# Kernel tuning notes

Hardware: AMD Instinct MI355X
Metric: run time of the kernel (lower is better)

The kernel has to match this reference:

```python
import jax, jax.numpy as jnp
import numpy as np

N_NODES = 50000
N_EDGES = 600000
IN_FEATS, HIDDEN, READOUT = 128, 128, 64
NUM_GRAPHS = 128
NEG_SLOPE = 0.01


def setup_inputs() -> dict:
    key = jax.random.key(0)
    ks = jax.random.split(key, 7)
    return {
        "x": jax.random.normal(ks[0], (N_NODES, IN_FEATS), dtype=jnp.float32),
        "edge_weight": jax.random.uniform(ks[1], (N_EDGES,), dtype=jnp.float32),
        "W1": jax.random.normal(ks[2], (IN_FEATS, HIDDEN), dtype=jnp.float32) * 0.05,
        "W2": jax.random.normal(ks[3], (HIDDEN, READOUT), dtype=jnp.float32) * 0.05,
        "src": jax.random.randint(ks[4], (N_EDGES,), 0, N_NODES, dtype=jnp.int32),
        "dst": jax.random.randint(ks[5], (N_EDGES,), 0, N_NODES, dtype=jnp.int32),
        "graph_ids": jax.random.randint(ks[6], (N_NODES,), 0, NUM_GRAPHS, dtype=jnp.int32),
        "num_graphs": NUM_GRAPHS,
    }


def reference(x, edge_weight, W1, W2, src, dst, graph_ids, num_graphs):
    n = x.shape[0]
    # DGL GraphConv norm='both': symmetric normalization from UNWEIGHTED degrees
    ones_e = jnp.ones(src.shape[0], dtype=x.dtype)
    out_deg = jnp.clip(jax.ops.segment_sum(ones_e, src, num_segments=n), 1.0)
    in_deg = jnp.clip(jax.ops.segment_sum(ones_e, dst, num_segments=n), 1.0)
    norm_src = out_deg ** -0.5  # applied on source side
    norm_dst = in_deg ** -0.5   # applied on destination side

    def gconv(h, W):
        # mult-W-first (in_feats >= out_feats path in DGL); math identical either way
        h = h @ W                               # [N, out]
        m = (h * norm_src[:, None])[src] * edge_weight[:, None]  # [E, out]
        agg = jax.ops.segment_sum(m, dst, num_segments=n)        # [N, out]
        return agg * norm_dst[:, None]

    h = jax.nn.leaky_relu(gconv(x, W1), NEG_SLOPE)
    h = jax.nn.leaky_relu(gconv(h, W2), NEG_SLOPE)

    # dgl.mean_nodes: per-graph mean over ragged node segments
    sums = jax.ops.segment_sum(h, graph_ids, num_segments=num_graphs)
    counts = jnp.clip(
        jax.ops.segment_sum(jnp.ones(n, dtype=h.dtype), graph_ids, num_segments=num_graphs),
        1.0,
    )
    return sums / counts[:, None]
```

## Files before the change

kernel.cpp:

```cpp
#include <hip/hip_runtime.h>


#define LB256 __launch_bounds__(256)
#define LB512 __launch_bounds__(512)

constexpr int RB = 128;
constexpr int CH = 8192;
constexpr int CHB = 13;
constexpr int SPLIT = 32;

__device__ __forceinline__ float leaky(float v) { return v > 0.f ? v : 0.01f * v; }

__global__ LB512 void k_hist(const int* __restrict__ src, const int* __restrict__ dst,
                             int* __restrict__ Pin, int* __restrict__ Pout,
                             int E, int epb) {
    __shared__ int hin[CH];
    __shared__ int hout[CH];
    const int c = blockIdx.x / SPLIT;
    const int s = blockIdx.x % SPLIT;
    const int t = threadIdx.x;
    const int4 z{0, 0, 0, 0};
    for (int i = t; i < CH / 4; i += 512) {
        ((int4*)hin)[i] = z;
        ((int4*)hout)[i] = z;
    }
    __syncthreads();

    const int base = c << CHB;
    const int e0 = s * epb;
    const int e1 = min(E, e0 + epb);
    if (e0 < e1) {
        const int nv = (e1 - e0) >> 2;
        const int4* d4 = (const int4*)(dst + e0);
        const int4* s4 = (const int4*)(src + e0);
        for (int i = t; i < nv; i += 512) {
            const int4 dd = d4[i], ss = s4[i];
            int v;
            v = dd.x - base; if ((unsigned)v < (unsigned)CH) atomicAdd(&hin[v], 1);
            v = dd.y - base; if ((unsigned)v < (unsigned)CH) atomicAdd(&hin[v], 1);
            v = dd.z - base; if ((unsigned)v < (unsigned)CH) atomicAdd(&hin[v], 1);
            v = dd.w - base; if ((unsigned)v < (unsigned)CH) atomicAdd(&hin[v], 1);
            v = ss.x - base; if ((unsigned)v < (unsigned)CH) atomicAdd(&hout[v], 1);
            v = ss.y - base; if ((unsigned)v < (unsigned)CH) atomicAdd(&hout[v], 1);
            v = ss.z - base; if ((unsigned)v < (unsigned)CH) atomicAdd(&hout[v], 1);
            v = ss.w - base; if ((unsigned)v < (unsigned)CH) atomicAdd(&hout[v], 1);
        }
        for (int e = e0 + (nv << 2) + t; e < e1; e += 512) {
            int v = dst[e] - base; if ((unsigned)v < (unsigned)CH) atomicAdd(&hin[v], 1);
            v = src[e] - base;     if ((unsigned)v < (unsigned)CH) atomicAdd(&hout[v], 1);
        }
    }
    __syncthreads();

    int4* pi = (int4*)&Pin[((size_t)c * SPLIT + s) * CH];
    int4* po = (int4*)&Pout[((size_t)c * SPLIT + s) * CH];
    for (int i = t; i < CH / 4; i += 512) {
        pi[i] = ((const int4*)hin)[i];
        po[i] = ((const int4*)hout)[i];
    }
}

__global__ LB256 void k_hreduce(int* __restrict__ Pin, const int* __restrict__ Pout,
                                int* __restrict__ cin, float* __restrict__ nin,
                                float* __restrict__ nout, int N) {
    const int i = blockIdx.x * 256 + threadIdx.x;
    if (i >= N) return;
    const int c = i >> CHB, l = i & (CH - 1);
    const size_t base = (size_t)c * SPLIT * CH + l;
    int acc = 0;
#pragma unroll
    for (int s = 0; s < SPLIT; ++s) {
        const size_t idx = base + (size_t)s * CH;
        const int v = Pin[idx];
        Pin[idx] = acc;
        acc += v;
    }
    int ao = 0;
#pragma unroll
    for (int s = 0; s < SPLIT; ++s) ao += Pout[base + (size_t)s * CH];
    cin[i] = acc;
    nin[i]  = rsqrtf(fmaxf((float)acc, 1.f));
    nout[i] = rsqrtf(fmaxf((float)ao, 1.f));
}

__device__ __forceinline__ int block_scan_incl(int v, int t) {
    const int lane = t & 63, w = t >> 6;
#pragma unroll
    for (int off = 1; off < 64; off <<= 1) {
        int n = __shfl_up(v, off);
        if (lane >= off) v += n;
    }
    __shared__ int wsum[4];
    if (lane == 63) wsum[w] = v;
    __syncthreads();
    int base = 0;
#pragma unroll
    for (int k = 0; k < 4; ++k)
        if (k < w) base += wsum[k];
    return v + base;
}

__global__ LB256 void k_scan1(const int* __restrict__ cnt, int* __restrict__ excl,
                              int* __restrict__ bsum, int N) {
    const int t = threadIdx.x, i = blockIdx.x * 256 + t;
    const int orig = (i < N) ? cnt[i] : 0;
    const int incl = block_scan_incl(orig, t);
    if (i < N) excl[i] = incl - orig;
    if (t == 255) bsum[blockIdx.x] = incl;
}

__global__ LB256 void k_scan2(const int* __restrict__ bsum, int* __restrict__ boff, int NB) {
    const int t = threadIdx.x;
    const int orig = (t < NB) ? bsum[t] : 0;
    const int incl = block_scan_incl(orig, t);
    if (t < NB) boff[t] = incl - orig;
}

__global__ LB256 void k_scan3(const int* __restrict__ excl, const int* __restrict__ boff,
                              int* __restrict__ row_off, int N) {
    const int i = blockIdx.x * 256 + threadIdx.x;
    if (i < N) row_off[i] = excl[i] + boff[blockIdx.x];
}

__global__ LB512 void k_fillr(const int* __restrict__ src, const int* __restrict__ dst,
                              const float* __restrict__ ew, const float* __restrict__ nout,
                              const int* __restrict__ Pin, const int* __restrict__ row_off,
                              int2* __restrict__ srw, int E, int epb) {
    __shared__ int h[CH];
    const int c = blockIdx.x / SPLIT;
    const int s = blockIdx.x % SPLIT;
    const int t = threadIdx.x;
    const int4 z{0, 0, 0, 0};
    for (int i = t; i < CH / 4; i += 512) ((int4*)h)[i] = z;
    __syncthreads();

    const int base = c << CHB;
    const int e0 = s * epb;
    const int e1 = min(E, e0 + epb);
    const int* off = &Pin[((size_t)c * SPLIT + s) * CH];
    if (e0 < e1) {
        const int nv = (e1 - e0) >> 2;
        const int4* d4 = (const int4*)(dst + e0);
        const int4* s4 = (const int4*)(src + e0);
        const float4* w4 = (const float4*)(ew + e0);
        for (int i = t; i < nv; i += 512) {
            const int4 dd = d4[i], ss = s4[i];
            const float4 ww = w4[i];
#define FILL1(D, S, W)                                                       \
            {                                                                \
                const int dl = (D) - base;                                   \
                if ((unsigned)dl < (unsigned)CH) {                           \
                    const int r = atomicAdd(&h[dl], 1);                      \
                    const int pos = row_off[D] + off[dl] + r;                \
                    srw[pos] = make_int2((S), __float_as_int(nout[S] * (W)));\
                }                                                            \
            }
            FILL1(dd.x, ss.x, ww.x)
            FILL1(dd.y, ss.y, ww.y)
            FILL1(dd.z, ss.z, ww.z)
            FILL1(dd.w, ss.w, ww.w)
        }
        for (int e = e0 + (nv << 2) + t; e < e1; e += 512) {
            FILL1(dst[e], src[e], ew[e])
        }
#undef FILL1
    }
}

template <int BN, int TN>
__global__ LB256 void k_gemm(const float* __restrict__ A, const float* __restrict__ W,
                             float* __restrict__ C, int N, int K) {
    constexpr int BM = 64, BK = 32;
    __shared__ float Xs[BM][BK + 1];
    __shared__ float Ws[BK][BN];

    const int tid = threadIdx.x;
    const int r0 = blockIdx.x * BM;
    const int ty = tid >> 4;
    const int tx = tid & 15;

    float acc[4][TN];
#pragma unroll
    for (int i = 0; i < 4; ++i)
#pragma unroll
        for (int j = 0; j < TN; ++j) acc[i][j] = 0.f;

    const int lrow = tid >> 2;
    const int lc = (tid & 3) * 4;
    const int kr = tid >> 3;

    for (int kc = 0; kc < K; kc += BK) {
        const int gr = r0 + lrow;
        if (gr < N) {
            *(float4*)&Xs[lrow][lc]      = *(const float4*)&A[(size_t)gr * K + kc + lc];
            *(float4*)&Xs[lrow][lc + 16] = *(const float4*)&A[(size_t)gr * K + kc + lc + 16];
        } else {
            *(float4*)&Xs[lrow][lc]      = float4{0.f, 0.f, 0.f, 0.f};
            *(float4*)&Xs[lrow][lc + 16] = float4{0.f, 0.f, 0.f, 0.f};
        }
#pragma unroll
        for (int j = 0; j < BN / 32; ++j) {
            const int c4 = (tid & 7) + j * 8;
            *(float4*)&Ws[kr][c4 * 4] =
                *(const float4*)&W[(size_t)(kc + kr) * BN + c4 * 4];
        }
        __syncthreads();

#pragma unroll
        for (int k = 0; k < BK; ++k) {
            float xv[4];
#pragma unroll
            for (int i = 0; i < 4; ++i) xv[i] = Xs[ty * 4 + i][k];
            float wv[TN];
#pragma unroll
            for (int j4 = 0; j4 < TN / 4; ++j4) {
                const float4 w4 = *(const float4*)&Ws[k][tx * TN + j4 * 4];
                wv[j4 * 4 + 0] = w4.x; wv[j4 * 4 + 1] = w4.y;
                wv[j4 * 4 + 2] = w4.z; wv[j4 * 4 + 3] = w4.w;
            }
#pragma unroll
            for (int i = 0; i < 4; ++i)
#pragma unroll
                for (int j = 0; j < TN; ++j) acc[i][j] = fmaf(xv[i], wv[j], acc[i][j]);
        }
        __syncthreads();
    }

#pragma unroll
    for (int i = 0; i < 4; ++i) {
        const int r = r0 + ty * 4 + i;
        if (r < N) {
#pragma unroll
            for (int j4 = 0; j4 < TN / 4; ++j4) {
                float4 o{acc[i][j4 * 4 + 0], acc[i][j4 * 4 + 1],
                         acc[i][j4 * 4 + 2], acc[i][j4 * 4 + 3]};
                *(float4*)&C[(size_t)r * BN + tx * TN + j4 * 4] = o;
            }
        }
    }
}

template <int F, int LANES>
__global__ LB256 void k_agg(const int* __restrict__ row_off, const int* __restrict__ cnt,
                            const int2* __restrict__ srw, const float* __restrict__ nin,
                            const float* __restrict__ h, float* __restrict__ out, int N) {
    const int node = blockIdx.x * (256 / LANES) + threadIdx.x / LANES;
    if (node >= N) return;
    const int lane = threadIdx.x % LANES;
    const int start = row_off[node], len = cnt[node];

    float4 accA{0.f, 0.f, 0.f, 0.f}, accB{0.f, 0.f, 0.f, 0.f};
    int j = 0;
    for (; j + 3 < len; j += 4) {
        const int b = start + j;
        const int2 r0_ = srw[b + 0], r1_ = srw[b + 1], r2_ = srw[b + 2], r3_ = srw[b + 3];
        const float c0 = __int_as_float(r0_.y), c1 = __int_as_float(r1_.y);
        const float c2 = __int_as_float(r2_.y), c3 = __int_as_float(r3_.y);
        const float4 v0 = *(const float4*)&h[(size_t)r0_.x * F + lane * 4];
        const float4 v1 = *(const float4*)&h[(size_t)r1_.x * F + lane * 4];
        const float4 v2 = *(const float4*)&h[(size_t)r2_.x * F + lane * 4];
        const float4 v3 = *(const float4*)&h[(size_t)r3_.x * F + lane * 4];
        accA.x = fmaf(c0, v0.x, fmaf(c1, v1.x, accA.x));
        accA.y = fmaf(c0, v0.y, fmaf(c1, v1.y, accA.y));
        accA.z = fmaf(c0, v0.z, fmaf(c1, v1.z, accA.z));
        accA.w = fmaf(c0, v0.w, fmaf(c1, v1.w, accA.w));
        accB.x = fmaf(c2, v2.x, fmaf(c3, v3.x, accB.x));
        accB.y = fmaf(c2, v2.y, fmaf(c3, v3.y, accB.y));
        accB.z = fmaf(c2, v2.z, fmaf(c3, v3.z, accB.z));
        accB.w = fmaf(c2, v2.w, fmaf(c3, v3.w, accB.w));
    }
    for (; j < len; ++j) {
        const int2 r0_ = srw[start + j];
        const float c0 = __int_as_float(r0_.y);
        const float4 v0 = *(const float4*)&h[(size_t)r0_.x * F + lane * 4];
        accA.x = fmaf(c0, v0.x, accA.x);
        accA.y = fmaf(c0, v0.y, accA.y);
        accA.z = fmaf(c0, v0.z, accA.z);
        accA.w = fmaf(c0, v0.w, accA.w);
    }
    const float nd = nin[node];
    float4 o{leaky((accA.x + accB.x) * nd), leaky((accA.y + accB.y) * nd),
             leaky((accA.z + accB.z) * nd), leaky((accA.w + accB.w) * nd)};
    *(float4*)&out[(size_t)node * F + lane * 4] = o;
}

__global__ LB256 void k_rpart(const float* __restrict__ h2, const int* __restrict__ gid,
                              float* __restrict__ part, int* __restrict__ pcnt,
                              int N, int npb) {
    __shared__ float lsum[128 * 64];
    __shared__ int lcnt[128];
    const int t = threadIdx.x;
    for (int i = t; i < 128 * 64; i += 256) lsum[i] = 0.f;
    if (t < 128) lcnt[t] = 0;
    __syncthreads();

    const int n0 = blockIdx.x * npb;
    const int n1 = min(N, n0 + npb);
    const int ty = t >> 6, lane = t & 63;
    for (int n = n0 + ty; n < n1; n += 4) {
        const int g = gid[n];
        atomicAdd(&lsum[g * 64 + lane], h2[(size_t)n * 64 + lane]);
        if (lane == 0) atomicAdd(&lcnt[g], 1);
    }
    __syncthreads();

    float* op = &part[(size_t)blockIdx.x * (128 * 64)];
    for (int i = t; i < 128 * 64; i += 256) op[i] = lsum[i];
    if (t < 128) pcnt[blockIdx.x * 128 + t] = lcnt[t];
}

__global__ LB256 void k_rfinal(const float* __restrict__ part, const int* __restrict__ pcnt,
                               float* __restrict__ out, int total) {
    const int i = blockIdx.x * 256 + threadIdx.x;
    if (i >= total) return;
    const int g = i >> 6;
    float s = 0.f;
    int c = 0;
#pragma unroll 4
    for (int b = 0; b < RB; ++b) {
        s += part[(size_t)b * (128 * 64) + i];
        c += pcnt[b * 128 + g];
    }
    out[i] = s / fmaxf((float)c, 1.f);
}

extern "C" void kernel_launch(void* const* d_in, const int* in_sizes, int n_in,
                              void* d_out, int out_size, void* d_ws, size_t ws_size,
                              hipStream_t stream) {
    const float* x   = (const float*)d_in[0];
    const float* ew  = (const float*)d_in[1];
    const float* W1  = (const float*)d_in[2];
    const float* W2  = (const float*)d_in[3];
    const int*   src = (const int*)d_in[4];
    const int*   dst = (const int*)d_in[5];
    const int*   gid = (const int*)d_in[6];

    const int N  = in_sizes[6];
    const int E  = in_sizes[4];
    const int NB = (N + 255) / 256;
    const int Na = (N + 63) & ~63;
    const int NCH = (N + CH - 1) / CH;
    const int epb = (((E + SPLIT - 1) / SPLIT) + 3) & ~3;

    char* p = (char*)d_ws;
    int*   cin     = (int*)p;                 p += (size_t)Na * 4;
    int*   excl    = (int*)p;                 p += (size_t)Na * 4;
    int*   bsum    = (int*)p;                 p += 256 * 4;
    int*   boff    = (int*)p;                 p += 256 * 4;
    int*   row_off = (int*)p;                 p += (size_t)Na * 4;
    float* nin     = (float*)p;               p += (size_t)Na * 4;
    float* nout    = (float*)p;               p += (size_t)Na * 4;
    int*   Pin     = (int*)p;                 p += (size_t)NCH * SPLIT * CH * 4;
    int*   Pout    = (int*)p;                 p += (size_t)NCH * SPLIT * CH * 4;
    int2*  srw     = (int2*)p;                p += (size_t)E * 8;
    float* t1      = (float*)p;               p += (size_t)N * 128 * 4;
    float* h1      = (float*)p;               p += (size_t)N * 128 * 4;
    float* h2      = (float*)p;               p += (size_t)N * 64 * 4;
    float* part    = (float*)p;               p += (size_t)RB * 128 * 64 * 4;
    int*   pcnt    = (int*)p;

    k_hist<<<NCH * SPLIT, 512, 0, stream>>>(src, dst, Pin, Pout, E, epb);
    k_hreduce<<<NB, 256, 0, stream>>>(Pin, Pout, cin, nin, nout, N);
    k_scan1<<<NB, 256, 0, stream>>>(cin, excl, bsum, N);
    k_scan2<<<1, 256, 0, stream>>>(bsum, boff, NB);
    k_scan3<<<NB, 256, 0, stream>>>(excl, boff, row_off, N);
    k_fillr<<<NCH * SPLIT, 512, 0, stream>>>(src, dst, ew, nout, Pin, row_off,
                                             srw, E, epb);

    k_gemm<128, 8><<<(N + 63) / 64, 256, 0, stream>>>(x, W1, t1, N, 128);
    k_agg<128, 32><<<(N + 7) / 8, 256, 0, stream>>>(row_off, cin, srw, nin, t1, h1, N);

    k_gemm<64, 4><<<(N + 63) / 64, 256, 0, stream>>>(h1, W2, t1, N, 128);
    k_agg<64, 16><<<(N + 15) / 16, 256, 0, stream>>>(row_off, cin, srw, nin, t1, h2, N);

    const int npb = (N + RB - 1) / RB;
    k_rpart<<<RB, 256, 0, stream>>>(h2, gid, part, pcnt, N, npb);
    k_rfinal<<<(128 * 64 + 255) / 256, 256, 0, stream>>>(part, pcnt, (float*)d_out,
                                                         128 * 64);
}
```

Before: 279.2 us.

## Fuse histogram reduce with block scan, transpose GEMM X tile, widen readout partials

Merges the per-node histogram reduction kernel with the first prefix-scan pass, which removes one launch and a global round trip of the counts. Stores the GEMM activation tile transposed in shared memory so each k-step reads four rows with one float4 load instead of four scalar loads, at the cost of scalar transposing stores. Doubles the number of readout partial blocks, which gives the final reduction more partials to sum. These are three unrelated changes bundled together.

```diff
diff --git a/kernel.cpp b/kernel.cpp
--- a/kernel.cpp
+++ b/kernel.cpp
@@ -4,7 +4,7 @@
 #define LB256 __launch_bounds__(256)
 #define LB512 __launch_bounds__(512)
 
-constexpr int RB = 128;
+constexpr int RB = 256;
 constexpr int CH = 8192;
 constexpr int CHB = 13;
 constexpr int SPLIT = 32;
@@ -60,29 +60,6 @@
     }
 }
 
-__global__ LB256 void k_hreduce(int* __restrict__ Pin, const int* __restrict__ Pout,
-                                int* __restrict__ cin, float* __restrict__ nin,
-                                float* __restrict__ nout, int N) {
-    const int i = blockIdx.x * 256 + threadIdx.x;
-    if (i >= N) return;
-    const int c = i >> CHB, l = i & (CH - 1);
-    const size_t base = (size_t)c * SPLIT * CH + l;
-    int acc = 0;
-#pragma unroll
-    for (int s = 0; s < SPLIT; ++s) {
-        const size_t idx = base + (size_t)s * CH;
-        const int v = Pin[idx];
-        Pin[idx] = acc;
-        acc += v;
-    }
-    int ao = 0;
-#pragma unroll
-    for (int s = 0; s < SPLIT; ++s) ao += Pout[base + (size_t)s * CH];
-    cin[i] = acc;
-    nin[i]  = rsqrtf(fmaxf((float)acc, 1.f));
-    nout[i] = rsqrtf(fmaxf((float)ao, 1.f));
-}
-
 __device__ __forceinline__ int block_scan_incl(int v, int t) {
     const int lane = t & 63, w = t >> 6;
 #pragma unroll
@@ -100,12 +77,31 @@
     return v + base;
 }
 
-__global__ LB256 void k_scan1(const int* __restrict__ cnt, int* __restrict__ excl,
-                              int* __restrict__ bsum, int N) {
+__global__ LB256 void k_hredscan(int* __restrict__ Pin, const int* __restrict__ Pout,
+                                 int* __restrict__ cin, float* __restrict__ nin,
+                                 float* __restrict__ nout, int* __restrict__ excl,
+                                 int* __restrict__ bsum, int N) {
     const int t = threadIdx.x, i = blockIdx.x * 256 + t;
-    const int orig = (i < N) ? cnt[i] : 0;
-    const int incl = block_scan_incl(orig, t);
-    if (i < N) excl[i] = incl - orig;
+    int acc = 0;
+    if (i < N) {
+        const int c = i >> CHB, l = i & (CH - 1);
+        const size_t base = (size_t)c * SPLIT * CH + l;
+#pragma unroll
+        for (int s = 0; s < SPLIT; ++s) {
+            const size_t idx = base + (size_t)s * CH;
+            const int v = Pin[idx];
+            Pin[idx] = acc;
+            acc += v;
+        }
+        int ao = 0;
+#pragma unroll
+        for (int s = 0; s < SPLIT; ++s) ao += Pout[base + (size_t)s * CH];
+        cin[i] = acc;
+        nin[i]  = rsqrtf(fmaxf((float)acc, 1.f));
+        nout[i] = rsqrtf(fmaxf((float)ao, 1.f));
+    }
+    const int incl = block_scan_incl(acc, t);
+    if (i < N) excl[i] = incl - acc;
     if (t == 255) bsum[blockIdx.x] = incl;
 }
 
@@ -171,7 +167,7 @@
 __global__ LB256 void k_gemm(const float* __restrict__ A, const float* __restrict__ W,
                              float* __restrict__ C, int N, int K) {
     constexpr int BM = 64, BK = 32;
-    __shared__ float Xs[BM][BK + 1];
+    __shared__ float Xs[BK][BM + 4];
     __shared__ float Ws[BK][BN];
 
     const int tid = threadIdx.x;
@@ -191,13 +187,15 @@
 
     for (int kc = 0; kc < K; kc += BK) {
         const int gr = r0 + lrow;
+        float4 v0{0.f, 0.f, 0.f, 0.f}, v1{0.f, 0.f, 0.f, 0.f};
         if (gr < N) {
-            *(float4*)&Xs[lrow][lc]      = *(const float4*)&A[(size_t)gr * K + kc + lc];
-            *(float4*)&Xs[lrow][lc + 16] = *(const float4*)&A[(size_t)gr * K + kc + lc + 16];
-        } else {
-            *(float4*)&Xs[lrow][lc]      = float4{0.f, 0.f, 0.f, 0.f};
-            *(float4*)&Xs[lrow][lc + 16] = float4{0.f, 0.f, 0.f, 0.f};
-        }
+            v0 = *(const float4*)&A[(size_t)gr * K + kc + lc];
+            v1 = *(const float4*)&A[(size_t)gr * K + kc + lc + 16];
+        }
+        Xs[lc + 0][lrow] = v0.x;  Xs[lc + 1][lrow] = v0.y;
+        Xs[lc + 2][lrow] = v0.z;  Xs[lc + 3][lrow] = v0.w;
+        Xs[lc + 16][lrow] = v1.x; Xs[lc + 17][lrow] = v1.y;
+        Xs[lc + 18][lrow] = v1.z; Xs[lc + 19][lrow] = v1.w;
 #pragma unroll
         for (int j = 0; j < BN / 32; ++j) {
             const int c4 = (tid & 7) + j * 8;
@@ -208,9 +206,8 @@
 
 #pragma unroll
         for (int k = 0; k < BK; ++k) {
-            float xv[4];
-#pragma unroll
-            for (int i = 0; i < 4; ++i) xv[i] = Xs[ty * 4 + i][k];
+            const float4 xq = *(const float4*)&Xs[k][ty * 4];
+            float xv[4] = {xq.x, xq.y, xq.z, xq.w};
             float wv[TN];
 #pragma unroll
             for (int j4 = 0; j4 < TN / 4; ++j4) {
@@ -360,8 +357,7 @@
     int*   pcnt    = (int*)p;
 
     k_hist<<<NCH * SPLIT, 512, 0, stream>>>(src, dst, Pin, Pout, E, epb);
-    k_hreduce<<<NB, 256, 0, stream>>>(Pin, Pout, cin, nin, nout, N);
-    k_scan1<<<NB, 256, 0, stream>>>(cin, excl, bsum, N);
+    k_hredscan<<<NB, 256, 0, stream>>>(Pin, Pout, cin, nin, nout, excl, bsum, N);
     k_scan2<<<1, 256, 0, stream>>>(bsum, boff, NB);
     k_scan3<<<NB, 256, 0, stream>>>(excl, boff, row_off, N);
     k_fillr<<<NCH * SPLIT, 512, 0, stream>>>(src, dst, ew, nout, Pin, row_off,
```

Result: faster. 273.7 us (-2.0%).
